# Optimization experiments

Measured on AMD Instinct MI355X. Metric: run time of the kernel, lower is better.

The kernel has to match this reference:

```python
import jax, jax.numpy as jnp
import numpy as np

EMB = 512
HEADS = 8
HEAD_DIM = EMB // HEADS


def setup_inputs() -> dict:
    key = jax.random.key(0)
    ks = jax.random.split(key, 6)
    b, t = 2, 4096
    x = jax.random.normal(ks[0], (b, t, EMB), dtype=jnp.float32)
    sc = 1.0 / np.sqrt(HEAD_DIM).astype(np.float32)
    Wq = jax.random.normal(ks[1], (HEAD_DIM, HEAD_DIM), dtype=jnp.float32) * sc
    Wk = jax.random.normal(ks[2], (HEAD_DIM, HEAD_DIM), dtype=jnp.float32) * sc
    Wv = jax.random.normal(ks[3], (HEAD_DIM, HEAD_DIM), dtype=jnp.float32) * sc
    Wu = jax.random.normal(ks[4], (EMB, EMB), dtype=jnp.float32) * (1.0 / np.sqrt(EMB).astype(np.float32))
    bu = jnp.zeros((EMB,), dtype=jnp.float32)
    return {"x": x, "Wq": Wq, "Wk": Wk, "Wv": Wv, "Wu": Wu, "bu": bu}


def reference(x, Wq, Wk, Wv, Wu, bu):
    b, t, e = x.shape
    s = Wq.shape[0]
    h = e // s
    xh = x.reshape(b, t, h, s)
    # torch Linear: y = x @ W.T (no bias for q/k/v)
    q = jnp.einsum('bthd,ed->bthe', xh, Wq)  # e here == s (head dim)
    k = jnp.einsum('bthd,ed->bthe', xh, Wk)
    v = jnp.einsum('bthd,ed->bthe', xh, Wv)
    # full [b,h,t,t] score matrix, scaled by sqrt(emb_dim) as in source
    dot = jnp.einsum('bqhd,bkhd->bhqk', q, k) / (e ** 0.5)
    att = jax.nn.softmax(dot, axis=-1)
    out = jnp.einsum('bhqk,bkhd->bqhd', att, v).reshape(b, t, e)
    return out @ Wu.T + bu
```

## Files before the change

### kernel.cpp

```cpp
#include <hip/hip_runtime.h>
#include <hip/hip_bf16.h>


#define T 4096
#define HEADS 8
#define HD 64
#define EMB 512
#define BATCH 2
#define BH (BATCH * HEADS)
#define NT (T / 64)

typedef __attribute__((ext_vector_type(8))) short short8;
typedef __attribute__((ext_vector_type(4))) float floatx4;

__device__ inline short f2bf(float f) {
  union { float f; unsigned u; } v; v.f = f;
  unsigned r = v.u + 0x7FFF + ((v.u >> 16) & 1);
  return (short)(r >> 16);
}

__device__ inline short8 pack8(float4 a, float4 b) {
  short8 o;
  o[0] = f2bf(a.x); o[1] = f2bf(a.y); o[2] = f2bf(a.z); o[3] = f2bf(a.w);
  o[4] = f2bf(b.x); o[5] = f2bf(b.y); o[6] = f2bf(b.z); o[7] = f2bf(b.w);
  return o;
}

__device__ inline short8 packbf(const float* p) {
  union { __hip_bfloat162 h[4]; short8 s; } u;
  float2 t;
  t.x = p[0]; t.y = p[1]; u.h[0] = __float22bfloat162_rn(t);
  t.x = p[2]; t.y = p[3]; u.h[1] = __float22bfloat162_rn(t);
  t.x = p[4]; t.y = p[5]; u.h[2] = __float22bfloat162_rn(t);
  t.x = p[6]; t.y = p[7]; u.h[3] = __float22bfloat162_rn(t);
  return u.s;
}

__device__ inline int swz(int row, int byte) {
  return (row * 128 + byte) ^ ((row & 7) << 4);
}

__global__ __launch_bounds__(256) void qkv_kernel(
    const float* __restrict__ x, const float* __restrict__ Wq,
    const float* __restrict__ Wk, const float* __restrict__ Wv,
    short* __restrict__ q_ws, short* __restrict__ k_ws, short* __restrict__ vt_ws) {
  __shared__ __align__(16) short xs[256 * 64];
  const int tid = threadIdx.x;
  const int lane = tid & 63;
  const int w = tid >> 6;
  const int g = lane >> 4, lr = lane & 15;
  const long rowbase = (long)blockIdx.x * 256;

  {
    const float4* xv = (const float4*)(x + (rowbase + tid) * 64);
    for (int c = 0; c < 8; ++c) {
      float4 a = xv[2 * c], b = xv[2 * c + 1];
      *(short8*)((char*)xs + swz(tid, c * 16)) = pack8(a, b);
    }
  }
  __syncthreads();

  const float* Ws[3] = {Wq, Wk, Wv};
  for (int m = 0; m < 3; ++m) {
    const float* W = Ws[m];
    for (int nt = 0; nt < 4; ++nt) {
      const int coln = nt * 16 + lr;
      const float4* wr0 = (const float4*)(W + coln * 64 + 8 * g);
      const float4* wr1 = (const float4*)(W + coln * 64 + 32 + 8 * g);
      short8 b0 = pack8(wr0[0], wr0[1]);
      short8 b1 = pack8(wr1[0], wr1[1]);
      for (int mr = 0; mr < 4; ++mr) {
        const int arow = w * 64 + mr * 16 + lr;
        short8 a0 = *(short8*)((char*)xs + swz(arow, g * 16));
        short8 a1 = *(short8*)((char*)xs + swz(arow, 64 + g * 16));
        floatx4 acc = 0;
        acc = __builtin_amdgcn_mfma_f32_16x16x32_bf16(a0, b0, acc, 0, 0, 0);
        acc = __builtin_amdgcn_mfma_f32_16x16x32_bf16(a1, b1, acc, 0, 0, 0);
        for (int jj = 0; jj < 4; ++jj) {
          long R = rowbase + w * 64 + mr * 16 + 4 * g + jj;
          int bb = (int)(R >> 15);
          int h = (int)(R & 7);
          int t = (int)((R >> 3) & 4095);
          if (m == 0)
            q_ws[(((long)(bb * HEADS + h) * T + t) * 64) + coln] = f2bf(acc[jj]);
          else if (m == 1)
            k_ws[(((long)(bb * HEADS + h) * T + t) * 64) + coln] = f2bf(acc[jj]);
          else {
            int tp = (t & ~31) | (((t >> 2) & 3) << 3) | (((t >> 4) & 1) << 2) | (t & 3);
            vt_ws[((long)(bb * HEADS + h) * 64 + coln) * T + tp] = f2bf(acc[jj]);
          }
        }
      }
    }
  }
}

__global__ __launch_bounds__(256) void attn_kernel(
    const short* __restrict__ q_ws, const short* __restrict__ k_ws,
    const short* __restrict__ vt_ws, short* __restrict__ o_ws) {
  __shared__ __align__(16) short Ks[2][64 * 64];
  __shared__ __align__(16) short Vs[2][64 * 64];
  const int tid = threadIdx.x, lane = tid & 63, w = tid >> 6;
  const int g = lane >> 4, lr = lane & 15;
  const int bh = blockIdx.y;
  const int q0 = blockIdx.x * 128;
  const short* Qp = q_ws + (long)bh * T * 64;
  const short* Kp = k_ws + (long)bh * T * 64;
  const short* Vt = vt_ws + (long)bh * 64 * T;

  const float c2 = 0.0441941738241592f * 1.4426950408889634f;

  short8 aq[2][2];
#pragma unroll
  for (int mt = 0; mt < 2; ++mt) {
    int r = q0 + w * 32 + mt * 16 + lr;
    aq[mt][0] = *(const short8*)(Qp + (long)r * 64 + g * 8);
    aq[mt][1] = *(const short8*)(Qp + (long)r * 64 + 32 + g * 8);
  }

  floatx4 acc[2][4];
#pragma unroll
  for (int mt = 0; mt < 2; ++mt)
#pragma unroll
    for (int dt = 0; dt < 4; ++dt) acc[mt][dt] = 0;
  float ellp[2] = {0.f, 0.f};

  const int srow = tid >> 2;
  const int sseg = (tid & 3) * 16;

  {
    const short8* ksrc = (const short8*)(Kp + (long)srow * 64 + sseg);
    short8 k0 = ksrc[0], k1 = ksrc[1];
    const short8* vsrc = (const short8*)(Vt + (long)srow * T + sseg);
    short8 v0 = vsrc[0], v1 = vsrc[1];
    *(short8*)((char*)Ks[0] + swz(srow, sseg * 2)) = k0;
    *(short8*)((char*)Ks[0] + swz(srow, sseg * 2 + 16)) = k1;
    *(short8*)((char*)Vs[0] + swz(srow, sseg * 2)) = v0;
    *(short8*)((char*)Vs[0] + swz(srow, sseg * 2 + 16)) = v1;
  }
  __syncthreads();

  for (int it = 0; it < NT; ++it) {
    const int cur = it & 1;
    const int nk = ((it + 1) & (NT - 1)) * 64;
    const short8* ksrc = (const short8*)(Kp + (long)(nk + srow) * 64 + sseg);
    short8 nk0 = ksrc[0], nk1 = ksrc[1];
    const short8* vsrc = (const short8*)(Vt + (long)srow * T + nk + sseg);
    short8 nv0 = vsrc[0], nv1 = vsrc[1];

    const char* KsB = (const char*)Ks[cur];
    const char* VsB = (const char*)Vs[cur];

    short8 kb[4][2], vb[4][2];
#pragma unroll
    for (int kt = 0; kt < 4; ++kt) {
      kb[kt][0] = *(const short8*)(KsB + swz(kt * 16 + lr, g * 16));
      kb[kt][1] = *(const short8*)(KsB + swz(kt * 16 + lr, 64 + g * 16));
    }
#pragma unroll
    for (int dt = 0; dt < 4; ++dt) {
      vb[dt][0] = *(const short8*)(VsB + swz(dt * 16 + lr, g * 16));
      vb[dt][1] = *(const short8*)(VsB + swz(dt * 16 + lr, 64 + g * 16));
    }

#pragma unroll
    for (int mt = 0; mt < 2; ++mt) {
      floatx4 s[4];
#pragma unroll
      for (int kt = 0; kt < 4; ++kt) {
        floatx4 z = 0;
        z = __builtin_amdgcn_mfma_f32_16x16x32_bf16(kb[kt][0], aq[mt][0], z, 0, 0, 0);
        z = __builtin_amdgcn_mfma_f32_16x16x32_bf16(kb[kt][1], aq[mt][1], z, 0, 0, 0);
        s[kt] = z;
      }
      float p[16];
#pragma unroll
      for (int kt = 0; kt < 4; ++kt)
#pragma unroll
        for (int r = 0; r < 4; ++r)
          p[kt * 4 + r] = __builtin_amdgcn_exp2f(fmaf(s[kt][r], c2, -3.0f));
#pragma unroll
      for (int e = 0; e < 16; ++e) ellp[mt] += p[e];
      short8 pa0 = packbf(p);
      short8 pa1 = packbf(p + 8);
#pragma unroll
      for (int dt = 0; dt < 4; ++dt) {
        acc[mt][dt] = __builtin_amdgcn_mfma_f32_16x16x32_bf16(pa0, vb[dt][0], acc[mt][dt], 0, 0, 0);
        acc[mt][dt] = __builtin_amdgcn_mfma_f32_16x16x32_bf16(pa1, vb[dt][1], acc[mt][dt], 0, 0, 0);
      }
    }

    char* KsN = (char*)Ks[cur ^ 1];
    char* VsN = (char*)Vs[cur ^ 1];
    *(short8*)(KsN + swz(srow, sseg * 2)) = nk0;
    *(short8*)(KsN + swz(srow, sseg * 2 + 16)) = nk1;
    *(short8*)(VsN + swz(srow, sseg * 2)) = nv0;
    *(short8*)(VsN + swz(srow, sseg * 2 + 16)) = nv1;
    __syncthreads();
  }

  float ef[2];
#pragma unroll
  for (int mt = 0; mt < 2; ++mt) {
    float e = ellp[mt];
    e += __shfl_xor(e, 16);
    e += __shfl_xor(e, 32);
    ef[mt] = e;
  }
  const int bb = bh >> 3, h = bh & 7;
#pragma unroll
  for (int mt = 0; mt < 2; ++mt) {
#pragma unroll
    for (int j = 0; j < 4; ++j) {
      float rl = 1.0f / __shfl(ef[mt], 4 * g + j);
      int trow = q0 + w * 32 + mt * 16 + 4 * g + j;
      long ob = ((long)(bb * T + trow)) * EMB + h * 64;
#pragma unroll
      for (int dt = 0; dt < 4; ++dt)
        o_ws[ob + dt * 16 + lr] = f2bf(acc[mt][dt][j] * rl);
    }
  }
}

__global__ __launch_bounds__(256) void proj_kernel(
    const short* __restrict__ o_ws, const float* __restrict__ Wu,
    const float* __restrict__ bu, float* __restrict__ out) {
  __shared__ __align__(16) short As[64 * 64];
  __shared__ __align__(16) short Bs[128 * 64];
  const int tid = threadIdx.x;
  const int lane = tid & 63, w = tid >> 6;
  const int g = lane >> 4, lr = lane & 15;
  const int m0 = blockIdx.x * 64;
  const int n0 = blockIdx.y * 128;

  floatx4 acc[8];
#pragma unroll
  for (int nt = 0; nt < 8; ++nt) acc[nt] = 0;

  for (int kc = 0; kc < EMB; kc += 64) {
    {
      int row = tid >> 2, kp = (tid & 3) * 16;
      const short8* src = (const short8*)(o_ws + (long)(m0 + row) * EMB + kc + kp);
      short8 v0 = src[0], v1 = src[1];
      *(short8*)((char*)As + swz(row, kp * 2)) = v0;
      *(short8*)((char*)As + swz(row, kp * 2 + 16)) = v1;
    }
#pragma unroll
    for (int nn = 0; nn < 2; ++nn) {
      int n = nn * 64 + (tid >> 2), kp = (tid & 3) * 16;
      const float4* src = (const float4*)(Wu + (long)(n0 + n) * EMB + kc + kp);
      *(short8*)((char*)Bs + swz(n, kp * 2)) = pack8(src[0], src[1]);
      *(short8*)((char*)Bs + swz(n, kp * 2 + 16)) = pack8(src[2], src[3]);
    }
    __syncthreads();

    int arow = w * 16 + lr;
    short8 a0 = *(short8*)((char*)As + swz(arow, g * 16));
    short8 a1 = *(short8*)((char*)As + swz(arow, 64 + g * 16));
#pragma unroll
    for (int nt = 0; nt < 8; ++nt) {
      int n = nt * 16 + lr;
      short8 b0 = *(short8*)((char*)Bs + swz(n, g * 16));
      short8 b1 = *(short8*)((char*)Bs + swz(n, 64 + g * 16));
      acc[nt] = __builtin_amdgcn_mfma_f32_16x16x32_bf16(a0, b0, acc[nt], 0, 0, 0);
      acc[nt] = __builtin_amdgcn_mfma_f32_16x16x32_bf16(a1, b1, acc[nt], 0, 0, 0);
    }
    __syncthreads();
  }

#pragma unroll
  for (int nt = 0; nt < 8; ++nt) {
    float bias = bu[n0 + nt * 16 + lr];
#pragma unroll
    for (int j = 0; j < 4; ++j) {
      int mrow = m0 + w * 16 + 4 * g + j;
      out[(long)mrow * EMB + n0 + nt * 16 + lr] = acc[nt][j] + bias;
    }
  }
}

extern "C" void kernel_launch(void* const* d_in, const int* in_sizes, int n_in,
                              void* d_out, int out_size, void* d_ws, size_t ws_size,
                              hipStream_t stream) {
  const float* x  = (const float*)d_in[0];
  const float* Wq = (const float*)d_in[1];
  const float* Wk = (const float*)d_in[2];
  const float* Wv = (const float*)d_in[3];
  const float* Wu = (const float*)d_in[4];
  const float* bu = (const float*)d_in[5];
  float* out = (float*)d_out;

  const long per = (long)BH * T * 64;
  short* q_ws  = (short*)d_ws;
  short* k_ws  = q_ws + per;
  short* vt_ws = k_ws + per;
  short* o_ws  = vt_ws + per;

  qkv_kernel<<<256, 256, 0, stream>>>(x, Wq, Wk, Wv, q_ws, k_ws, vt_ws);
  attn_kernel<<<dim3(T / 128, BH), 256, 0, stream>>>(q_ws, k_ws, vt_ws, o_ws);
  proj_kernel<<<dim3(BATCH * T / 64, EMB / 128), 256, 0, stream>>>(o_ws, Wu, bu, out);
}
```

Before: 135.2 us.

## Coalesce QKV and projection stores via transposed MFMA and LDS staging

The QKV kernel now processes 128 rows per block, so twice as many blocks launch. It swaps the MFMA operands so that each lane holds four consecutive output columns. Q and K results are staged through a swizzled LDS buffer and then written to global memory as 16-byte vectors, and V^T stores become row-contiguous per lane. The projection kernel also swaps operands so that each lane writes a float4 of output, with a vectorized bias add. The goal is to replace scattered 2-byte and 4-byte stores with coalesced wide stores, at the cost of extra LDS traffic and syncs in the QKV kernel.

```diff
diff --git a/kernel.cpp b/kernel.cpp
--- a/kernel.cpp
+++ b/kernel.cpp
@@ -11,6 +11,7 @@
 #define NT (T / 64)
 
 typedef __attribute__((ext_vector_type(8))) short short8;
+typedef __attribute__((ext_vector_type(4))) short short4v;
 typedef __attribute__((ext_vector_type(4))) float floatx4;
 
 __device__ inline short f2bf(float f) {
@@ -44,18 +45,21 @@
     const float* __restrict__ x, const float* __restrict__ Wq,
     const float* __restrict__ Wk, const float* __restrict__ Wv,
     short* __restrict__ q_ws, short* __restrict__ k_ws, short* __restrict__ vt_ws) {
-  __shared__ __align__(16) short xs[256 * 64];
+  __shared__ __align__(16) short xs[128 * 64];
+  __shared__ __align__(16) short ob[128 * 64];
   const int tid = threadIdx.x;
   const int lane = tid & 63;
   const int w = tid >> 6;
   const int g = lane >> 4, lr = lane & 15;
-  const long rowbase = (long)blockIdx.x * 256;
+  const long rowbase = (long)blockIdx.x * 128;
 
   {
-    const float4* xv = (const float4*)(x + (rowbase + tid) * 64);
-    for (int c = 0; c < 8; ++c) {
+    int row = tid >> 1, hf = tid & 1;
+    const float4* xv = (const float4*)(x + (rowbase + row) * 64 + hf * 32);
+#pragma unroll
+    for (int c = 0; c < 4; ++c) {
       float4 a = xv[2 * c], b = xv[2 * c + 1];
-      *(short8*)((char*)xs + swz(tid, c * 16)) = pack8(a, b);
+      *(short8*)((char*)xs + swz(row, hf * 64 + c * 16)) = pack8(a, b);
     }
   }
   __syncthreads();
@@ -64,33 +68,54 @@
   for (int m = 0; m < 3; ++m) {
     const float* W = Ws[m];
     for (int nt = 0; nt < 4; ++nt) {
-      const int coln = nt * 16 + lr;
-      const float4* wr0 = (const float4*)(W + coln * 64 + 8 * g);
-      const float4* wr1 = (const float4*)(W + coln * 64 + 32 + 8 * g);
+      const int coln_a = nt * 16 + lr;
+      const float4* wr0 = (const float4*)(W + coln_a * 64 + 8 * g);
+      const float4* wr1 = (const float4*)(W + coln_a * 64 + 32 + 8 * g);
       short8 b0 = pack8(wr0[0], wr0[1]);
       short8 b1 = pack8(wr1[0], wr1[1]);
-      for (int mr = 0; mr < 4; ++mr) {
-        const int arow = w * 64 + mr * 16 + lr;
+      for (int mr = 0; mr < 2; ++mr) {
+        const int arow = w * 32 + mr * 16 + lr;
         short8 a0 = *(short8*)((char*)xs + swz(arow, g * 16));
         short8 a1 = *(short8*)((char*)xs + swz(arow, 64 + g * 16));
         floatx4 acc = 0;
-        acc = __builtin_amdgcn_mfma_f32_16x16x32_bf16(a0, b0, acc, 0, 0, 0);
-        acc = __builtin_amdgcn_mfma_f32_16x16x32_bf16(a1, b1, acc, 0, 0, 0);
-        for (int jj = 0; jj < 4; ++jj) {
-          long R = rowbase + w * 64 + mr * 16 + 4 * g + jj;
+        acc = __builtin_amdgcn_mfma_f32_16x16x32_bf16(b0, a0, acc, 0, 0, 0);
+        acc = __builtin_amdgcn_mfma_f32_16x16x32_bf16(b1, a1, acc, 0, 0, 0);
+        if (m < 2) {
+          short4v pk;
+          pk[0] = f2bf(acc[0]); pk[1] = f2bf(acc[1]);
+          pk[2] = f2bf(acc[2]); pk[3] = f2bf(acc[3]);
+          *(short4v*)((char*)ob + swz(w * 32 + mr * 16 + lr, 32 * nt + 8 * g)) = pk;
+        } else {
+          long R = rowbase + w * 32 + mr * 16 + lr;
           int bb = (int)(R >> 15);
           int h = (int)(R & 7);
           int t = (int)((R >> 3) & 4095);
-          if (m == 0)
-            q_ws[(((long)(bb * HEADS + h) * T + t) * 64) + coln] = f2bf(acc[jj]);
-          else if (m == 1)
-            k_ws[(((long)(bb * HEADS + h) * T + t) * 64) + coln] = f2bf(acc[jj]);
-          else {
-            int tp = (t & ~31) | (((t >> 2) & 3) << 3) | (((t >> 4) & 1) << 2) | (t & 3);
+          int tp = (t & ~31) | (((t >> 2) & 3) << 3) | (((t >> 4) & 1) << 2) | (t & 3);
+#pragma unroll
+          for (int jj = 0; jj < 4; ++jj) {
+            int coln = nt * 16 + 4 * g + jj;
             vt_ws[((long)(bb * HEADS + h) * 64 + coln) * T + tp] = f2bf(acc[jj]);
           }
         }
       }
+    }
+    if (m < 2) {
+      short* dst_ws = (m == 0) ? q_ws : k_ws;
+      __syncthreads();
+      {
+        int row = tid >> 1, hf = tid & 1;
+        long R = rowbase + row;
+        int bb = (int)(R >> 15);
+        int h = (int)(R & 7);
+        int t = (int)((R >> 3) & 4095);
+        short* dst = dst_ws + ((long)(bb * HEADS + h) * T + t) * 64 + hf * 32;
+#pragma unroll
+        for (int c = 0; c < 4; ++c) {
+          short8 v = *(short8*)((char*)ob + swz(row, hf * 64 + c * 16));
+          *(short8*)(dst + c * 8) = v;
+        }
+      }
+      __syncthreads();
     }
   }
 }
@@ -214,10 +239,10 @@
     for (int j = 0; j < 4; ++j) {
       float rl = 1.0f / __shfl(ef[mt], 4 * g + j);
       int trow = q0 + w * 32 + mt * 16 + 4 * g + j;
-      long ob = ((long)(bb * T + trow)) * EMB + h * 64;
+      long ob2 = ((long)(bb * T + trow)) * EMB + h * 64;
 #pragma unroll
       for (int dt = 0; dt < 4; ++dt)
-        o_ws[ob + dt * 16 + lr] = f2bf(acc[mt][dt][j] * rl);
+        o_ws[ob2 + dt * 16 + lr] = f2bf(acc[mt][dt][j] * rl);
     }
   }
 }
@@ -262,20 +287,22 @@
       int n = nt * 16 + lr;
       short8 b0 = *(short8*)((char*)Bs + swz(n, g * 16));
       short8 b1 = *(short8*)((char*)Bs + swz(n, 64 + g * 16));
-      acc[nt] = __builtin_amdgcn_mfma_f32_16x16x32_bf16(a0, b0, acc[nt], 0, 0, 0);
-      acc[nt] = __builtin_amdgcn_mfma_f32_16x16x32_bf16(a1, b1, acc[nt], 0, 0, 0);
+      acc[nt] = __builtin_amdgcn_mfma_f32_16x16x32_bf16(b0, a0, acc[nt], 0, 0, 0);
+      acc[nt] = __builtin_amdgcn_mfma_f32_16x16x32_bf16(b1, a1, acc[nt], 0, 0, 0);
     }
     __syncthreads();
   }
 
+  const int mrow = m0 + w * 16 + lr;
 #pragma unroll
   for (int nt = 0; nt < 8; ++nt) {
-    float bias = bu[n0 + nt * 16 + lr];
-#pragma unroll
-    for (int j = 0; j < 4; ++j) {
-      int mrow = m0 + w * 16 + 4 * g + j;
-      out[(long)mrow * EMB + n0 + nt * 16 + lr] = acc[nt][j] + bias;
-    }
+    float4 bias = *(const float4*)(bu + n0 + nt * 16 + 4 * g);
+    float4 o;
+    o.x = acc[nt][0] + bias.x;
+    o.y = acc[nt][1] + bias.y;
+    o.z = acc[nt][2] + bias.z;
+    o.w = acc[nt][3] + bias.w;
+    *(float4*)(out + (long)mrow * EMB + n0 + nt * 16 + 4 * g) = o;
   }
 }
 
@@ -296,7 +323,7 @@
   short* vt_ws = k_ws + per;
   short* o_ws  = vt_ws + per;
 
-  qkv_kernel<<<256, 256, 0, stream>>>(x, Wq, Wk, Wv, q_ws, k_ws, vt_ws);
+  qkv_kernel<<<512, 256, 0, stream>>>(x, Wq, Wk, Wv, q_ws, k_ws, vt_ws);
   attn_kernel<<<dim3(T / 128, BH), 256, 0, stream>>>(q_ws, k_ws, vt_ws, o_ws);
   proj_kernel<<<dim3(BATCH * T / 64, EMB / 128), 256, 0, stream>>>(o_ws, Wu, bu, out);
 }
```

New measurement: 132.7 us. About the same (-1.9%).
